# Kernel optimization log

Hardware: AMD Instinct MI355X
Metric: run time of the kernel (lower is better)

Reference implementation:

```python
import jax, jax.numpy as jnp
import numpy as np
import math

D_MODEL = 1024
RPN_D = 256
SUP_HW = 20  # support feature map is 20x20 -> 400 tokens


def _positional_encoding(max_len, d_model):
    pos = np.arange(max_len, dtype=np.float32)[:, None]
    div = np.exp(np.arange(0, d_model, 2, dtype=np.float32) * -(math.log(10000.0) / float(d_model)))
    pe = np.zeros((max_len, d_model), dtype=np.float32)
    pe[:, 0::2] = np.sin(pos * div)
    pe[:, 1::2] = np.cos(pos * div)
    return jnp.asarray(pe)


def setup_inputs() -> dict:
    key = jax.random.key(0)
    ks = jax.random.split(key, 6)
    B, S, H = 4, 5, 4
    fh, fw = 64, 64
    base_feat = jax.random.normal(ks[0], (B, D_MODEL, fh, fw), dtype=jnp.float32)
    support_feat = jax.random.normal(ks[1], (B, S, D_MODEL, SUP_HW, SUP_HW), dtype=jnp.float32)
    Qw = jax.random.normal(ks[2], (H, RPN_D, D_MODEL), dtype=jnp.float32) * 0.01
    Qb = jnp.zeros((H, RPN_D), dtype=jnp.float32)
    Kw = jax.random.normal(ks[3], (H, RPN_D, D_MODEL), dtype=jnp.float32) * 0.01
    Kb = jnp.zeros((H, RPN_D), dtype=jnp.float32)
    Mw = jax.random.normal(ks[4], (D_MODEL, H * D_MODEL), dtype=jnp.float32) * 0.02
    Mb = jnp.zeros((D_MODEL,), dtype=jnp.float32)
    return {"base_feat": base_feat, "support_feat": support_feat,
            "Qw": Qw, "Qb": Qb, "Kw": Kw, "Kb": Kb, "Mw": Mw, "Mb": Mb}


def reference(base_feat, support_feat, Qw, Qb, Kw, Kb, Mw, Mb):
    B, C, fh, fw = base_feat.shape
    S = support_feat.shape[1]
    H = Qw.shape[0]
    Lq = fh * fw
    Lk = SUP_HW * SUP_HW

    # support_mat: [S, B, Lk, C]  (transpose(0,1) then flatten spatial, then transpose)
    support_mat = jnp.transpose(support_feat, (1, 0, 2, 3, 4)).reshape(S, B, C, Lk)
    support_mat = jnp.transpose(support_mat, (0, 1, 3, 2))
    # query_mat: [B, Lq, C]
    query_mat = jnp.transpose(base_feat.reshape(B, C, Lq), (0, 2, 1))

    pe = _positional_encoding(400, D_MODEL)[:Lk]  # [Lk, C]
    s_mat = support_mat + pe[None, None]          # [S, B, Lk, C]

    # per-head projections (q is independent of shot, compute once)
    q = jnp.einsum('blc,hdc->hbld', query_mat, Qw) + Qb[:, None, None, :]   # [H,B,Lq,d]
    k = jnp.einsum('sbkc,hdc->hsbkd', s_mat, Kw) + Kb[:, None, None, None, :]  # [H,S,B,Lk,d]

    scores = jnp.einsum('hbld,hsbkd->hsblk', q, k) / math.sqrt(RPN_D)  # [H,S,B,Lq,Lk]
    attn = jax.nn.softmax(scores, axis=-1)
    z = jnp.einsum('hsblk,sbkc->hsblc', attn, s_mat)  # [H,S,B,Lq,C]

    # shot_mode == 'mean'
    z = jnp.mean(z, axis=1)  # [H,B,Lq,C]

    # concat heads along feature dim (head order preserved): [B,Lq,H*C]
    att = jnp.transpose(z, (1, 2, 0, 3)).reshape(B, Lq, H * C)
    att = jax.nn.relu(att @ Mw.T + Mb)  # [B,Lq,C]

    att = jnp.transpose(att, (0, 2, 1)).reshape(B, C, fh, fw)
    # attention_type == 'product'
    correlation_feat = base_feat * att
    return correlation_feat
```

## Files before the change

kernel.cpp:

```cpp
#include <hip/hip_runtime.h>
#include <stdint.h>

#define DEVI __device__ __forceinline__

typedef __attribute__((ext_vector_type(8))) short bf16x8;
typedef __attribute__((ext_vector_type(4))) float f32x4;
typedef __attribute__((ext_vector_type(4))) unsigned short us4;
typedef unsigned short u16;

constexpr int B_ = 4, S_ = 5, H_ = 4, C_ = 1024, D_ = 256;
constexpr int LQ = 4096, LK = 400, LKP = 448;

DEVI u16 f2b(float f){
  uint32_t x = __float_as_uint(f);
  uint32_t r = (x + 0x7FFFu + ((x >> 16) & 1u)) >> 16;
  return (u16)r;
}

typedef __attribute__((address_space(1))) const void ASG;
typedef __attribute__((address_space(3))) void ASL;
DEVI void gload16(const void* g, void* l){
  __builtin_amdgcn_global_load_lds((ASG*)g, (ASL*)l, 16, 0, 0);
}

__global__ __launch_bounds__(256) void k_cvt(const float* __restrict__ s, u16* __restrict__ d, int n4){
  int i = blockIdx.x*256 + threadIdx.x;
  if (i >= n4) return;
  float4 v = ((const float4*)s)[i];
  us4 o; o.x = f2b(v.x); o.y = f2b(v.y); o.z = f2b(v.z); o.w = f2b(v.w);
  *(us4*)(d + (size_t)i*4) = o;
}

__global__ __launch_bounds__(256) void k_transpose_x(const float* __restrict__ base, u16* __restrict__ Xb){
  __shared__ float t[32][33];
  int l0 = blockIdx.x*32, c0 = blockIdx.y*32, b = blockIdx.z;
  int tx = threadIdx.x & 31, ty = threadIdx.x >> 5;
  const float* src = base + ((size_t)b*C_ + c0)*LQ + l0;
  #pragma unroll
  for (int i=0;i<4;i++){ int cc = ty + i*8; t[cc][tx] = src[(size_t)cc*LQ + tx]; }
  __syncthreads();
  u16* dst = Xb + ((size_t)b*LQ + l0)*C_ + c0;
  #pragma unroll
  for (int i=0;i<4;i++){ int ll = ty + i*8; dst[(size_t)ll*C_ + tx] = f2b(t[tx][ll]); }
}

__global__ __launch_bounds__(256) void k_build_smat(const float* __restrict__ sup, u16* __restrict__ kc){
  __shared__ float t[32][33];
  int p0 = blockIdx.x*32, c0 = blockIdx.y*32;
  int s = blockIdx.z / B_, b = blockIdx.z % B_;
  int tx = threadIdx.x & 31, ty = threadIdx.x >> 5;
  const float* src = sup + ((size_t)(b*S_ + s)*C_ + c0)*LK + p0;
  #pragma unroll
  for (int i=0;i<4;i++){
    int cc = ty + i*8;
    int p = p0 + tx;
    int c = c0 + cc;
    float v = 0.f;
    if (p < LK){
      v = src[(size_t)cc*LK + tx];
      float dv = expf(-(float)(c & ~1) * (9.210340371976184f / 1024.f));
      float arg = (float)p * dv;
      v += (c & 1) ? cosf(arg) : sinf(arg);
    }
    t[cc][tx] = v;
  }
  __syncthreads();
  u16* dkc = kc + ((size_t)((s*B_ + b)*LKP + p0))*C_ + c0;
  #pragma unroll
  for (int i=0;i<4;i++){ int pp = ty + i*8; dkc[(size_t)pp*C_ + tx] = f2b(t[tx][pp]); }
}

DEVI void stage_half(const u16* P, int64_t ld, u16* dst, int wid, int r8, int s8){
  #pragma unroll
  for (int it=0; it<2; ++it){
    int ck = wid + it*8;
    gload16(P + (size_t)(ck*8 + r8)*ld + s8*8, dst + ck*512);
  }
}
DEVI bf16x8 ldsread(const u16* base, int row, int kk, int lane){
  int sl = ((kk<<2) + (lane>>4)) ^ (row & 7);
  return *(const bf16x8*)&base[row*64 + sl*8];
}

template<int CEPI, bool FIRST, bool FINAL, bool BIAS>
__global__ __launch_bounds__(512,1) void k8(
    const u16* __restrict__ A, const u16* __restrict__ Bm, void* __restrict__ Cm,
    const float* __restrict__ bias, const float* __restrict__ basep, const float* __restrict__ Mb,
    int tilesM, int64_t lda, int64_t ldb, int64_t ldc, int NT,
    int bdiv, int64_t aS0, int64_t aS1, int64_t bS0, int64_t bS1,
    int64_t cS0, int64_t cS1, int64_t aZ, int64_t bZ, int64_t cZ,
    int biasS0, float scale, int Nmax, int Mmax, int swz){
  __shared__ __align__(16) u16 lds[2][2][16384];
  int tid = threadIdx.x, lane = tid & 63, wid = tid >> 6;
  int bx = blockIdx.x;
  int mt, ntile;
  if (swz == 2){ int x = bx & 7, j = bx >> 3; mt = 2*x + (j >> 2); ntile = j & 3; }
  else {
    if (swz == 1) bx = (bx & 7) * (gridDim.x >> 3) + (bx >> 3);
    mt = bx % tilesM; ntile = bx / tilesM;
  }
  int z = blockIdx.y, i0 = z / bdiv, i1 = z % bdiv;
  int iz = blockIdx.z;
  const u16* Ab = A + i0*aS0 + i1*aS1 + iz*aZ + (size_t)mt*256*lda;
  const u16* Bb = Bm + i0*bS0 + i1*bS1 + iz*bZ + (size_t)ntile*256*ldb;
  int r8 = lane >> 3, s8 = (lane & 7) ^ r8;
  int wr = wid >> 2, wc = wid & 3;

  f32x4 acc[8][4];
  #pragma unroll
  for (int i=0;i<8;i++)
    #pragma unroll
    for (int j=0;j<4;j++) acc[i][j] = (f32x4){0.f,0.f,0.f,0.f};

  const u16 *ApS = Ab, *BpS = Bb;
  stage_half(ApS,                   lda, &lds[0][0][0],    wid, r8, s8);
  stage_half(ApS + (size_t)128*lda, lda, &lds[0][0][8192], wid, r8, s8);
  stage_half(BpS,                   ldb, &lds[0][1][0],    wid, r8, s8);
  stage_half(BpS + (size_t)128*ldb, ldb, &lds[0][1][8192], wid, r8, s8);
  ApS += 64; BpS += 64;

  for (int t = 0; t < NT; ++t){
    int cur = t & 1, nxt = cur ^ 1;
    bool pf = (t + 1 < NT);
    const u16* lA = &lds[cur][0][0];
    const u16* lB = &lds[cur][1][0];
    u16* sA = &lds[nxt][0][0];
    u16* sB = &lds[nxt][1][0];
    if (pf){
      stage_half(ApS,                   lda, sA,        wid, r8, s8);
      stage_half(ApS + (size_t)128*lda, lda, sA + 8192, wid, r8, s8);
      asm volatile("s_waitcnt vmcnt(4)" ::: "memory");
    } else {
      asm volatile("s_waitcnt vmcnt(0)" ::: "memory");
    }
    asm volatile("s_barrier" ::: "memory");

    bf16x8 bfr[4][2];
    #pragma unroll
    for (int jn=0;jn<4;jn++)
      #pragma unroll
      for (int kk=0;kk<2;kk++)
        bfr[jn][kk] = ldsread(lB, wc*64 + jn*16 + (lane & 15), kk, lane);

    #pragma unroll
    for (int p = 0; p < 4; ++p){
      bf16x8 af[2][2];
      #pragma unroll
      for (int dm=0;dm<2;dm++)
        #pragma unroll
        for (int kk=0;kk<2;kk++)
          af[dm][kk] = ldsread(lA, wr*128 + (p*2+dm)*16 + (lane & 15), kk, lane);
      __builtin_amdgcn_s_setprio(1);
      #pragma unroll
      for (int dm=0;dm<2;dm++)
        #pragma unroll
        for (int jn=0;jn<4;jn++)
          #pragma unroll
          for (int kk=0;kk<2;kk++)
            acc[p*2+dm][jn] = __builtin_amdgcn_mfma_f32_16x16x32_bf16(af[dm][kk], bfr[jn][kk], acc[p*2+dm][jn], 0,0,0);
      __builtin_amdgcn_s_setprio(0);
      if (p == 0 && pf) stage_half(BpS,                   ldb, sB,        wid, r8, s8);
      if (p == 1 && pf) stage_half(BpS + (size_t)128*ldb, ldb, sB + 8192, wid, r8, s8);
    }
    asm volatile("s_barrier" ::: "memory");
    if (pf){ ApS += 64; BpS += 64; }
  }

  int g = lane >> 4, c16 = lane & 15;
  if constexpr (CEPI == 0){
    u16* Cb = (u16*)Cm + i0*cS0 + i1*cS1 + iz*cZ;
    #pragma unroll
    for (int jn=0;jn<4;jn++){
      int n = ntile*256 + wc*64 + jn*16 + c16;
      if (n >= Nmax) continue;
      float bv = 0.f;
      if (BIAS) bv = bias[(size_t)i0*biasS0 + n];
      #pragma unroll
      for (int im=0;im<8;im++){
        int m = mt*256 + wr*128 + im*16 + g*4;
        if (m >= Mmax) continue;
        #pragma unroll
        for (int r=0;r<4;r++)
          Cb[(size_t)(m + r)*ldc + n] = f2b((acc[im][jn][r] + bv)*scale);
      }
    }
  } else {
    float* Cb = (float*)Cm + i0*cS0 + i1*cS1 + iz*cZ;
    const float* Bs = basep + i0*cS0 + i1*cS1 + iz*cZ;
    #pragma unroll
    for (int jn=0;jn<4;jn++){
      int n = ntile*256 + wc*64 + jn*16 + c16;
      float mbv = 0.f;
      if (FINAL) mbv = Mb[n];
      #pragma unroll
      for (int im=0;im<8;im++){
        int m = mt*256 + wr*128 + im*16 + g*4;
        float* p = Cb + (size_t)n*ldc + m;
        float4 v;
        v.x = acc[im][jn][0]; v.y = acc[im][jn][1]; v.z = acc[im][jn][2]; v.w = acc[im][jn][3];
        if (!FIRST){
          float4 old = *(const float4*)p;
          v.x += old.x; v.y += old.y; v.z += old.z; v.w += old.w;
        }
        if (FINAL){
          float4 bs = *(const float4*)(Bs + (size_t)n*ldc + m);
          v.x = bs.x * fmaxf(0.2f*v.x + mbv, 0.f);
          v.y = bs.y * fmaxf(0.2f*v.y + mbv, 0.f);
          v.z = bs.z * fmaxf(0.2f*v.z + mbv, 0.f);
          v.w = bs.w * fmaxf(0.2f*v.w + mbv, 0.f);
        }
        *(float4*)p = v;
      }
    }
  }
}

__global__ __launch_bounds__(512,1) void k_scores(
    const u16* __restrict__ qws, const u16* __restrict__ kws,
    u16* __restrict__ attn, int h0, int KVP, int padw, int nz){
  __shared__ __align__(16) u16 lQ[128*64];
  __shared__ __align__(16) u16 lK[448*64];
  __shared__ float red[128][4];
  __shared__ float rowv[128];
  int tid = threadIdx.x, lane = tid & 63, wid = tid >> 6;
  int m0 = blockIdx.x * 128;
  int b = blockIdx.y;
  int zz = blockIdx.z;
  int s = zz % 5, h = h0 + zz / 5;
  const u16* Qp = qws + ((size_t)(h*B_ + b)*LQ + m0)*D_;
  const u16* Kp = kws + ((size_t)((h*S_ + s)*B_ + b))*((size_t)LKP*D_);
  int r8 = lane >> 3, s8 = (lane & 7) ^ r8;
  int c16 = lane & 15, g = lane >> 4;
  int wm2 = wid >> 2, wkv = wid & 3;

  f32x4 acc[4][7];
  #pragma unroll
  for (int m=0;m<4;m++)
    #pragma unroll
    for (int tt=0;tt<7;tt++) acc[m][tt] = (f32x4){0.f,0.f,0.f,0.f};

  for (int k0 = 0; k0 < 256; k0 += 64){
    __syncthreads();
    #pragma unroll
    for (int c = 0; c < 2; ++c){
      int cc = wid + c*8;
      gload16(Qp + (size_t)(cc*8 + r8)*D_ + k0 + s8*8, &lQ[cc*512]);
    }
    #pragma unroll
    for (int i = 0; i < 7; ++i){
      int ck = wid + i*8;
      gload16(Kp + (size_t)(ck*8 + r8)*D_ + k0 + s8*8, &lK[ck*512]);
    }
    __syncthreads();

    bf16x8 af[4][2];
    #pragma unroll
    for (int m=0;m<4;m++)
      #pragma unroll
      for (int kk=0;kk<2;kk++)
        af[m][kk] = ldsread(lQ, wm2*64 + m*16 + c16, kk, lane);
    __builtin_amdgcn_s_setprio(1);
    #pragma unroll
    for (int tt=0;tt<7;tt++)
      #pragma unroll
      for (int kk=0;kk<2;kk++){
        bf16x8 bf = ldsread(lK, wkv*112 + tt*16 + c16, kk, lane);
        #pragma unroll
        for (int m=0;m<4;m++)
          acc[m][tt] = __builtin_amdgcn_mfma_f32_16x16x32_bf16(af[m][kk], bf, acc[m][tt], 0,0,0);
      }
    __builtin_amdgcn_s_setprio(0);
  }

  float pmax[4][4];
  if (wkv == 3){
    #pragma unroll
    for (int m=0;m<4;m++)
      #pragma unroll
      for (int r=0;r<4;r++){
        float v = acc[m][0][r];
        v = fmaxf(v, acc[m][1][r]); v = fmaxf(v, acc[m][2][r]); v = fmaxf(v, acc[m][3][r]);
        pmax[m][r] = v;
      }
  } else {
    #pragma unroll
    for (int m=0;m<4;m++)
      #pragma unroll
      for (int r=0;r<4;r++){
        float v = acc[m][0][r];
        v = fmaxf(v, acc[m][1][r]); v = fmaxf(v, acc[m][2][r]); v = fmaxf(v, acc[m][3][r]);
        v = fmaxf(v, acc[m][4][r]); v = fmaxf(v, acc[m][5][r]); v = fmaxf(v, acc[m][6][r]);
        pmax[m][r] = v;
      }
  }
  #pragma unroll
  for (int m=0;m<4;m++)
    #pragma unroll
    for (int r=0;r<4;r++){
      pmax[m][r] = fmaxf(pmax[m][r], __shfl_xor(pmax[m][r], 1));
      pmax[m][r] = fmaxf(pmax[m][r], __shfl_xor(pmax[m][r], 2));
      pmax[m][r] = fmaxf(pmax[m][r], __shfl_xor(pmax[m][r], 4));
      pmax[m][r] = fmaxf(pmax[m][r], __shfl_xor(pmax[m][r], 8));
    }
  if (c16 == 0){
    #pragma unroll
    for (int m=0;m<4;m++)
      #pragma unroll
      for (int r=0;r<4;r++)
        red[wm2*64 + m*16 + g*4 + r][wkv] = pmax[m][r];
  }
  __syncthreads();
  if (tid < 128)
    rowv[tid] = fmaxf(fmaxf(red[tid][0], red[tid][1]), fmaxf(red[tid][2], red[tid][3]));
  __syncthreads();
  float mxr[4][4];
  #pragma unroll
  for (int m=0;m<4;m++)
    #pragma unroll
    for (int r=0;r<4;r++) mxr[m][r] = rowv[wm2*64 + m*16 + g*4 + r];

  float ps[4][4];
  #pragma unroll
  for (int m=0;m<4;m++)
    #pragma unroll
    for (int r=0;r<4;r++) ps[m][r] = 0.f;
  if (wkv == 3){
    #pragma unroll
    for (int tt=0;tt<4;tt++)
      #pragma unroll
      for (int m=0;m<4;m++)
        #pragma unroll
        for (int r=0;r<4;r++){
          float e = __expf(acc[m][tt][r] - mxr[m][r]);
          acc[m][tt][r] = e; ps[m][r] += e;
        }
  } else {
    #pragma unroll
    for (int tt=0;tt<7;tt++)
      #pragma unroll
      for (int m=0;m<4;m++)
        #pragma unroll
        for (int r=0;r<4;r++){
          float e = __expf(acc[m][tt][r] - mxr[m][r]);
          acc[m][tt][r] = e; ps[m][r] += e;
        }
  }
  #pragma unroll
  for (int m=0;m<4;m++)
    #pragma unroll
    for (int r=0;r<4;r++){
      ps[m][r] += __shfl_xor(ps[m][r], 1);
      ps[m][r] += __shfl_xor(ps[m][r], 2);
      ps[m][r] += __shfl_xor(ps[m][r], 4);
      ps[m][r] += __shfl_xor(ps[m][r], 8);
    }
  if (c16 == 0){
    #pragma unroll
    for (int m=0;m<4;m++)
      #pragma unroll
      for (int r=0;r<4;r++)
        red[wm2*64 + m*16 + g*4 + r][wkv] = ps[m][r];
  }
  __syncthreads();
  if (tid < 128)
    rowv[tid] = 1.f / (red[tid][0] + red[tid][1] + red[tid][2] + red[tid][3]);
  __syncthreads();

  u16* ap = attn + ((size_t)b*LQ + m0)*KVP + (size_t)zz*400;
  if (wkv == 3){
    #pragma unroll
    for (int m=0;m<4;m++)
      #pragma unroll
      for (int r=0;r<4;r++){
        int rowl = wm2*64 + m*16 + g*4 + r;
        float rs = rowv[rowl];
        #pragma unroll
        for (int tt=0;tt<4;tt++)
          ap[(size_t)rowl*KVP + wkv*112 + tt*16 + c16] = f2b(acc[m][tt][r] * rs);
      }
  } else {
    #pragma unroll
    for (int m=0;m<4;m++)
      #pragma unroll
      for (int r=0;r<4;r++){
        int rowl = wm2*64 + m*16 + g*4 + r;
        float rs = rowv[rowl];
        #pragma unroll
        for (int tt=0;tt<7;tt++)
          ap[(size_t)rowl*KVP + wkv*112 + tt*16 + c16] = f2b(acc[m][tt][r] * rs);
      }
  }
  if (zz == nz - 1 && padw > 0){
    u16* base2 = attn + ((size_t)b*LQ + m0)*KVP + (KVP - padw);
    int total = 128 * padw;
    for (int i = tid; i < total; i += 512){
      int rr = i / padw, cc = i % padw;
      base2[(size_t)rr*KVP + cc] = 0;
    }
  }
}

extern "C" void kernel_launch(void* const* d_in, const int* in_sizes, int n_in,
                              void* d_out, int out_size, void* d_ws, size_t ws_size,
                              hipStream_t stream){
  const float* base = (const float*)d_in[0];
  const float* sup  = (const float*)d_in[1];
  const float* Qw   = (const float*)d_in[2];
  const float* Qb   = (const float*)d_in[3];
  const float* Kw   = (const float*)d_in[4];
  const float* Kb   = (const float*)d_in[5];
  const float* Mw   = (const float*)d_in[6];
  const float* Mb   = (const float*)d_in[7];
  float* out = (float*)d_out;
  char* ws = (char*)d_ws;

  const int GH = (ws_size >= 247988224ull) ? 2 : 1;
  const int NG = H_ / GH;
  const int NZ = GH * 5;
  const int KVP = (NZ*400 + 63) & ~63;
  const int NT = KVP / 64;
  const int PADW = KVP - NZ*400;

  u16* wQw = (u16*)(ws + 0);
  u16* wKw = (u16*)(ws + 2097152);
  u16* wMw = (u16*)(ws + 4194304);
  u16* wKC = (u16*)(ws + 12582912);
  u16* wK  = (u16*)(ws + 30932992);
  u16* wQ  = (u16*)(ws + 49283072);
  u16* wVt = (u16*)(ws + 82837504);
  u16* wAT = (u16*)(ws + 82837504 + (size_t)B_*C_*KVP*2);
  u16* wXb = wAT;

  const int BIG = 1 << 30;

  k_cvt<<<1024, 256, 0, stream>>>(Qw, wQw, 262144);
  k_cvt<<<1024, 256, 0, stream>>>(Kw, wKw, 262144);
  k_cvt<<<4096, 256, 0, stream>>>(Mw, wMw, 1048576);
  k_transpose_x<<<dim3(128, 32, 4), 256, 0, stream>>>(base, wXb);
  k_build_smat<<<dim3(14, 32, 20), 256, 0, stream>>>(sup, wKC);

  k8<0,false,false,true><<<dim3(2, 80, 1), 512, 0, stream>>>(
      wKC, wKw, wK, Kb, nullptr, nullptr,
      2, C_, C_, D_, 16,
      20, 0, (int64_t)LKP*C_, (int64_t)D_*C_, 0,
      (int64_t)S_*B_*LKP*D_, (int64_t)LKP*D_, 0, 0, 0,
      D_, 1.f, BIG, LKP, 0);

  k8<0,false,false,true><<<dim3(16, 16, 1), 512, 0, stream>>>(
      wXb, wQw, wQ, Qb, nullptr, nullptr,
      16, C_, C_, D_, 16,
      4, 0, (int64_t)LQ*C_, (int64_t)D_*C_, 0,
      (int64_t)B_*LQ*D_, (int64_t)LQ*D_, 0, 0, 0,
      D_, 1.f/16.f, BIG, BIG, 1);

  for (int g = 0; g < NG; ++g){
    k8<0,false,false,false><<<dim3(8, NZ, 4), 512, 0, stream>>>(
        wMw + (size_t)(g*GH)*C_, wKC, wVt, nullptr, nullptr, nullptr,
        4, (int64_t)H_*C_, C_, KVP, 16,
        5, (int64_t)C_, 0, 0, (int64_t)B_*LKP*C_,
        2000, 400, 0, (int64_t)LKP*C_, (int64_t)C_*KVP,
        0, 1.f, 400, BIG, 0);

    k_scores<<<dim3(32, 4, NZ), 512, 0, stream>>>(wQ, wK, wAT, g*GH, KVP, PADW, NZ);

    if (g == 0 && NG > 1){
      k8<1,true,false,false><<<dim3(64, 4, 1), 512, 0, stream>>>(
          wAT, wVt, out, nullptr, base, Mb,
          16, KVP, KVP, LQ, NT,
          1, (int64_t)LQ*KVP, 0, (int64_t)C_*KVP, 0,
          (int64_t)C_*LQ, 0, 0, 0, 0,
          0, 1.f, BIG, BIG, 2);
    } else if (g == NG - 1){
      k8<1,false,true,false><<<dim3(64, 4, 1), 512, 0, stream>>>(
          wAT, wVt, out, nullptr, base, Mb,
          16, KVP, KVP, LQ, NT,
          1, (int64_t)LQ*KVP, 0, (int64_t)C_*KVP, 0,
          (int64_t)C_*LQ, 0, 0, 0, 0,
          0, 1.f, BIG, BIG, 2);
    } else {
      k8<1,false,false,false><<<dim3(64, 4, 1), 512, 0, stream>>>(
          wAT, wVt, out, nullptr, base, Mb,
          16, KVP, KVP, LQ, NT,
          1, (int64_t)LQ*KVP, 0, (int64_t)C_*KVP, 0,
          (int64_t)C_*LQ, 0, 0, 0, 0,
          0, 1.f, BIG, BIG, 2);
    }
  }
}
```

Baseline: 728.5 us.

## Pack support tokens densely, double-buffer score loads, and merge weight conversions

The support-token layout drops the per-shot padding to 448 rows and packs the 5 shots contiguously as 2000 rows per batch. This lets the K-projection and value-projection GEMMs run as larger batched launches with fewer wasted padded rows. The scores kernel now double-buffers its Q/K LDS tiles, prefetching the next k-slice while MFMAs run on the current one, using explicit vmcnt waits and barriers. The three weight-conversion launches are merged into one kernel. The cost is doubled LDS in the scores kernel and K tiles that now read past 400 rows into the next shot's data, which relies on masking later.

```diff
diff --git a/kernel.cpp b/kernel.cpp
--- a/kernel.cpp
+++ b/kernel.cpp
@@ -9,7 +9,7 @@
 typedef unsigned short u16;
 
 constexpr int B_ = 4, S_ = 5, H_ = 4, C_ = 1024, D_ = 256;
-constexpr int LQ = 4096, LK = 400, LKP = 448;
+constexpr int LQ = 4096, LK = 400;
 
 DEVI u16 f2b(float f){
   uint32_t x = __float_as_uint(f);
@@ -23,12 +23,19 @@
   __builtin_amdgcn_global_load_lds((ASG*)g, (ASL*)l, 16, 0, 0);
 }
 
-__global__ __launch_bounds__(256) void k_cvt(const float* __restrict__ s, u16* __restrict__ d, int n4){
+__global__ __launch_bounds__(256) void k_cvt3(
+    const float* __restrict__ s0, u16* __restrict__ d0, int n0,
+    const float* __restrict__ s1, u16* __restrict__ d1, int n1,
+    const float* __restrict__ s2, u16* __restrict__ d2, int n2){
   int i = blockIdx.x*256 + threadIdx.x;
-  if (i >= n4) return;
-  float4 v = ((const float4*)s)[i];
+  const float* s; u16* d; int idx;
+  if (i < n0){ s = s0; d = d0; idx = i; }
+  else if (i < n0 + n1){ s = s1; d = d1; idx = i - n0; }
+  else if (i < n0 + n1 + n2){ s = s2; d = d2; idx = i - n0 - n1; }
+  else return;
+  float4 v = ((const float4*)s)[idx];
   us4 o; o.x = f2b(v.x); o.y = f2b(v.y); o.z = f2b(v.z); o.w = f2b(v.w);
-  *(us4*)(d + (size_t)i*4) = o;
+  *(us4*)(d + (size_t)idx*4) = o;
 }
 
 __global__ __launch_bounds__(256) void k_transpose_x(const float* __restrict__ base, u16* __restrict__ Xb){
@@ -65,9 +72,12 @@
     t[cc][tx] = v;
   }
   __syncthreads();
-  u16* dkc = kc + ((size_t)((s*B_ + b)*LKP + p0))*C_ + c0;
-  #pragma unroll
-  for (int i=0;i<4;i++){ int pp = ty + i*8; dkc[(size_t)pp*C_ + tx] = f2b(t[tx][pp]); }
+  u16* dkc = kc + ((size_t)((b*S_ + s)*400 + p0))*C_ + c0;
+  #pragma unroll
+  for (int i=0;i<4;i++){
+    int pp = ty + i*8;
+    if (p0 + pp < 400) dkc[(size_t)pp*C_ + tx] = f2b(t[tx][pp]);
+  }
 }
 
 DEVI void stage_half(const u16* P, int64_t ld, u16* dst, int wid, int r8, int s8){
@@ -218,8 +228,8 @@
 __global__ __launch_bounds__(512,1) void k_scores(
     const u16* __restrict__ qws, const u16* __restrict__ kws,
     u16* __restrict__ attn, int h0, int KVP, int padw, int nz){
-  __shared__ __align__(16) u16 lQ[128*64];
-  __shared__ __align__(16) u16 lK[448*64];
+  __shared__ __align__(16) u16 lQ[2][128*64];
+  __shared__ __align__(16) u16 lK[2][448*64];
   __shared__ float red[128][4];
   __shared__ float rowv[128];
   int tid = threadIdx.x, lane = tid & 63, wid = tid >> 6;
@@ -228,7 +238,7 @@
   int zz = blockIdx.z;
   int s = zz % 5, h = h0 + zz / 5;
   const u16* Qp = qws + ((size_t)(h*B_ + b)*LQ + m0)*D_;
-  const u16* Kp = kws + ((size_t)((h*S_ + s)*B_ + b))*((size_t)LKP*D_);
+  const u16* Kp = kws + ((size_t)((h*B_ + b)*2000 + s*400))*D_;
   int r8 = lane >> 3, s8 = (lane & 7) ^ r8;
   int c16 = lane & 15, g = lane >> 4;
   int wm2 = wid >> 2, wkv = wid & 3;
@@ -239,37 +249,56 @@
     #pragma unroll
     for (int tt=0;tt<7;tt++) acc[m][tt] = (f32x4){0.f,0.f,0.f,0.f};
 
-  for (int k0 = 0; k0 < 256; k0 += 64){
-    __syncthreads();
-    #pragma unroll
-    for (int c = 0; c < 2; ++c){
-      int cc = wid + c*8;
-      gload16(Qp + (size_t)(cc*8 + r8)*D_ + k0 + s8*8, &lQ[cc*512]);
-    }
-    #pragma unroll
-    for (int i = 0; i < 7; ++i){
-      int ck = wid + i*8;
-      gload16(Kp + (size_t)(ck*8 + r8)*D_ + k0 + s8*8, &lK[ck*512]);
-    }
-    __syncthreads();
-
+  #pragma unroll
+  for (int c = 0; c < 2; ++c){
+    int cc = wid + c*8;
+    gload16(Qp + (size_t)(cc*8 + r8)*D_ + s8*8, &lQ[0][cc*512]);
+  }
+  #pragma unroll
+  for (int i = 0; i < 7; ++i){
+    int ck = wid + i*8;
+    gload16(Kp + (size_t)(ck*8 + r8)*D_ + s8*8, &lK[0][ck*512]);
+  }
+
+  for (int t = 0; t < 4; ++t){
+    if (t < 3){
+      int k1 = (t+1)*64;
+      int nb = (t+1) & 1;
+      #pragma unroll
+      for (int c = 0; c < 2; ++c){
+        int cc = wid + c*8;
+        gload16(Qp + (size_t)(cc*8 + r8)*D_ + k1 + s8*8, &lQ[nb][cc*512]);
+      }
+      #pragma unroll
+      for (int i = 0; i < 7; ++i){
+        int ck = wid + i*8;
+        gload16(Kp + (size_t)(ck*8 + r8)*D_ + k1 + s8*8, &lK[nb][ck*512]);
+      }
+      asm volatile("s_waitcnt vmcnt(9)" ::: "memory");
+    } else {
+      asm volatile("s_waitcnt vmcnt(0)" ::: "memory");
+    }
+    asm volatile("s_barrier" ::: "memory");
+    const u16* lq = &lQ[t & 1][0];
+    const u16* lk = &lK[t & 1][0];
     bf16x8 af[4][2];
     #pragma unroll
     for (int m=0;m<4;m++)
       #pragma unroll
       for (int kk=0;kk<2;kk++)
-        af[m][kk] = ldsread(lQ, wm2*64 + m*16 + c16, kk, lane);
+        af[m][kk] = ldsread(lq, wm2*64 + m*16 + c16, kk, lane);
     __builtin_amdgcn_s_setprio(1);
     #pragma unroll
     for (int tt=0;tt<7;tt++)
       #pragma unroll
       for (int kk=0;kk<2;kk++){
-        bf16x8 bf = ldsread(lK, wkv*112 + tt*16 + c16, kk, lane);
+        bf16x8 bf = ldsread(lk, wkv*112 + tt*16 + c16, kk, lane);
         #pragma unroll
         for (int m=0;m<4;m++)
           acc[m][tt] = __builtin_amdgcn_mfma_f32_16x16x32_bf16(af[m][kk], bf, acc[m][tt], 0,0,0);
       }
     __builtin_amdgcn_s_setprio(0);
+    asm volatile("s_barrier" ::: "memory");
   }
 
   float pmax[4][4];
@@ -433,18 +462,16 @@
 
   const int BIG = 1 << 30;
 
-  k_cvt<<<1024, 256, 0, stream>>>(Qw, wQw, 262144);
-  k_cvt<<<1024, 256, 0, stream>>>(Kw, wKw, 262144);
-  k_cvt<<<4096, 256, 0, stream>>>(Mw, wMw, 1048576);
+  k_cvt3<<<6144, 256, 0, stream>>>(Qw, wQw, 262144, Kw, wKw, 262144, Mw, wMw, 1048576);
   k_transpose_x<<<dim3(128, 32, 4), 256, 0, stream>>>(base, wXb);
-  k_build_smat<<<dim3(14, 32, 20), 256, 0, stream>>>(sup, wKC);
-
-  k8<0,false,false,true><<<dim3(2, 80, 1), 512, 0, stream>>>(
+  k_build_smat<<<dim3(13, 32, 20), 256, 0, stream>>>(sup, wKC);
+
+  k8<0,false,false,true><<<dim3(8, 16, 1), 512, 0, stream>>>(
       wKC, wKw, wK, Kb, nullptr, nullptr,
-      2, C_, C_, D_, 16,
-      20, 0, (int64_t)LKP*C_, (int64_t)D_*C_, 0,
-      (int64_t)S_*B_*LKP*D_, (int64_t)LKP*D_, 0, 0, 0,
-      D_, 1.f, BIG, LKP, 0);
+      8, C_, C_, D_, 16,
+      4, 0, (int64_t)S_*400*C_, (int64_t)D_*C_, 0,
+      (int64_t)B_*2000*D_, (int64_t)2000*D_, 0, 0, 0,
+      D_, 1.f, BIG, 2000, 0);
 
   k8<0,false,false,true><<<dim3(16, 16, 1), 512, 0, stream>>>(
       wXb, wQw, wQ, Qb, nullptr, nullptr,
@@ -454,12 +481,12 @@
       D_, 1.f/16.f, BIG, BIG, 1);
 
   for (int g = 0; g < NG; ++g){
-    k8<0,false,false,false><<<dim3(8, NZ, 4), 512, 0, stream>>>(
+    k8<0,false,false,false><<<dim3(32, GH, 4), 512, 0, stream>>>(
         wMw + (size_t)(g*GH)*C_, wKC, wVt, nullptr, nullptr, nullptr,
         4, (int64_t)H_*C_, C_, KVP, 16,
-        5, (int64_t)C_, 0, 0, (int64_t)B_*LKP*C_,
-        2000, 400, 0, (int64_t)LKP*C_, (int64_t)C_*KVP,
-        0, 1.f, 400, BIG, 0);
+        1, (int64_t)C_, 0, 0, 0,
+        2000, 0, 0, (int64_t)S_*400*C_, (int64_t)C_*KVP,
+        0, 1.f, 2000, BIG, 0);
 
     k_scores<<<dim3(32, 4, NZ), 512, 0, stream>>>(wQ, wK, wAT, g*GH, KVP, PADW, NZ);
 
```

Result: faster. 676.6 us (-7.1%).
